# Optimization experiments

Hardware: AMD Instinct MI355X
Metric: run time of the kernel (lower is better)

The kernel has to match this reference:

```python
import jax, jax.numpy as jnp
import numpy as np

N_NODES = 100000
N_EDGES = 640000
IN_DIM, HID_DIM, OUT_DIM = 128, 64, 32


def setup_inputs() -> dict:
    key = jax.random.key(0)
    ks = jax.random.split(key, 8)
    x = jax.random.normal(ks[0], (N_NODES, IN_DIM), dtype=jnp.float32)
    edge_index = jax.random.randint(ks[1], (2, N_EDGES), 0, N_NODES, dtype=jnp.int64)
    # SAGEConv params: lin_l (applied to aggregated neighbors, has bias),
    # lin_r (applied to root node, no bias) -- PyG defaults.
    s1 = 1.0 / np.sqrt(IN_DIM)
    s2 = 1.0 / np.sqrt(HID_DIM)
    W1l = jax.random.uniform(ks[2], (HID_DIM, IN_DIM), jnp.float32, -s1, s1)
    b1 = jax.random.uniform(ks[3], (HID_DIM,), jnp.float32, -s1, s1)
    W1r = jax.random.uniform(ks[4], (HID_DIM, IN_DIM), jnp.float32, -s1, s1)
    W2l = jax.random.uniform(ks[5], (OUT_DIM, HID_DIM), jnp.float32, -s2, s2)
    b2 = jax.random.uniform(ks[6], (OUT_DIM,), jnp.float32, -s2, s2)
    W2r = jax.random.uniform(ks[7], (OUT_DIM, HID_DIM), jnp.float32, -s2, s2)
    return {"x": x, "edge_index": edge_index,
            "W1l": W1l, "b1": b1, "W1r": W1r,
            "W2l": W2l, "b2": b2, "W2r": W2r}


def _sage_conv(x, src, dst, Wl, b, Wr, num_nodes):
    # mean aggregation of source features onto destination nodes
    msg = x[src]                                                # [E, d]
    agg = jax.ops.segment_sum(msg, dst, num_segments=num_nodes)  # [N, d]
    cnt = jax.ops.segment_sum(jnp.ones((src.shape[0],), x.dtype), dst,
                              num_segments=num_nodes)            # [N]
    agg = agg / jnp.maximum(cnt, 1.0)[:, None]
    # out = lin_l(mean_neighbors) + lin_r(x)
    return agg @ Wl.T + b + x @ Wr.T


def reference(x, edge_index, W1l, b1, W1r, W2l, b2, W2r):
    src, dst = edge_index[0], edge_index[1]
    n = x.shape[0]
    h = jax.nn.relu(_sage_conv(x, src, dst, W1l, b1, W1r, n))
    out = _sage_conv(h, src, dst, W2l, b2, W2r, n)
    return out
```

## Files before the change

kernel.cpp:

```cpp
#include <hip/hip_runtime.h>
#include <hip/hip_bf16.h>

typedef __hip_bfloat16 bf16;
typedef __attribute__((ext_vector_type(8))) short short8;
typedef __attribute__((ext_vector_type(4))) float f32x4;

#define N_NODES 100000
#define N_EDGES 640000
#define NSB 98
#define N_TILES 6250

__device__ __forceinline__ float bf2f(short s) {
    union { float f; unsigned u; } u;
    u.u = ((unsigned)(unsigned short)s) << 16;
    return u.f;
}
__device__ __forceinline__ short f2s(float f) {
    union { bf16 b; short s; } u;
    u.b = __float2bfloat16(f);
    return u.s;
}

__device__ __forceinline__ int detect_is64(const int* __restrict__ idx) {
    int lane = threadIdx.x & 63;
    int v = idx[2 * (lane & 31) + 1];
    return __ballot(v == 0) == ~0ULL;
}
__device__ __forceinline__ int detect_f32(const unsigned* __restrict__ xw) {
    int lane = threadIdx.x & 63;
    unsigned e = (xw[lane] >> 7) & 0xFFu;
    int inr = (e >= 0x20u && e <= 0x4Fu);
    return __popcll(__ballot(inr)) < 48;
}

__device__ __forceinline__ void decode8(
        const int* __restrict__ eidx, int is64, int e0, int E,
        int (&ss)[8], int (&dd)[8]) {
    if (is64) {
        int4 a0 = *(const int4*)&eidx[2 * e0];
        int4 a1 = *(const int4*)&eidx[2 * e0 + 4];
        int4 a2 = *(const int4*)&eidx[2 * e0 + 8];
        int4 a3 = *(const int4*)&eidx[2 * e0 + 12];
        int4 b0 = *(const int4*)&eidx[2 * (E + e0)];
        int4 b1 = *(const int4*)&eidx[2 * (E + e0) + 4];
        int4 b2 = *(const int4*)&eidx[2 * (E + e0) + 8];
        int4 b3 = *(const int4*)&eidx[2 * (E + e0) + 12];
        ss[0] = a0.x; ss[1] = a0.z; ss[2] = a1.x; ss[3] = a1.z;
        ss[4] = a2.x; ss[5] = a2.z; ss[6] = a3.x; ss[7] = a3.z;
        dd[0] = b0.x; dd[1] = b0.z; dd[2] = b1.x; dd[3] = b1.z;
        dd[4] = b2.x; dd[5] = b2.z; dd[6] = b3.x; dd[7] = b3.z;
    } else {
        int4 s0 = *(const int4*)&eidx[e0];
        int4 s1 = *(const int4*)&eidx[e0 + 4];
        int4 d0 = *(const int4*)&eidx[E + e0];
        int4 d1 = *(const int4*)&eidx[E + e0 + 4];
        ss[0] = s0.x; ss[1] = s0.y; ss[2] = s0.z; ss[3] = s0.w;
        ss[4] = s1.x; ss[5] = s1.y; ss[6] = s1.z; ss[7] = s1.w;
        dd[0] = d0.x; dd[1] = d0.y; dd[2] = d0.z; dd[3] = d0.w;
        dd[4] = d1.x; dd[5] = d1.y; dd[6] = d1.z; dd[7] = d1.w;
    }
}

__global__ __launch_bounds__(256) void hist_kernel(
        const int* __restrict__ eidx, int* __restrict__ deg,
        int* __restrict__ rank, int E, int N) {
    const int is64 = detect_is64(eidx);
    int e0 = (blockIdx.x * 256 + threadIdx.x) * 8;
    if (e0 >= E) return;
    int ss[8], dd[8], rk[8];
    decode8(eidx, is64, e0, E, ss, dd);
#pragma unroll
    for (int c = 0; c < 8; ++c) {
        bool ok = (unsigned)ss[c] < (unsigned)N && (unsigned)dd[c] < (unsigned)N;
        rk[c] = ok ? atomicAdd(&deg[dd[c]], 1) : 0;
    }
    *(int4*)&rank[e0]     = make_int4(rk[0], rk[1], rk[2], rk[3]);
    *(int4*)&rank[e0 + 4] = make_int4(rk[4], rk[5], rk[6], rk[7]);
}

__global__ __launch_bounds__(256) void scan_partial_kernel(
        const int* __restrict__ deg, int* __restrict__ off,
        int* __restrict__ bsum, int N) {
    __shared__ int ss[256];
    const int tid = threadIdx.x, blk = blockIdx.x;
    const int base = blk * 1024 + tid * 4;
    int v[4], s = 0;
    if (base + 3 < N) {
        int4 dv = *(const int4*)&deg[base];
        v[0] = dv.x; v[1] = dv.y; v[2] = dv.z; v[3] = dv.w;
    } else {
#pragma unroll
        for (int c = 0; c < 4; ++c) v[c] = (base + c < N) ? deg[base + c] : 0;
    }
#pragma unroll
    for (int c = 0; c < 4; ++c) s += v[c];
    ss[tid] = s; __syncthreads();
    for (int o = 1; o < 256; o <<= 1) {
        int t = (tid >= o) ? ss[tid - o] : 0;
        __syncthreads();
        ss[tid] += t;
        __syncthreads();
    }
    int run = ss[tid] - s;
    if (tid == 255) bsum[blk] = ss[255];
#pragma unroll
    for (int c = 0; c < 4; ++c) {
        if (base + c < N) off[base + c] = run;
        run += v[c];
    }
}

__global__ __launch_bounds__(256) void scan_add_kernel(
        int* __restrict__ off, const int* __restrict__ bsum, int N) {
    __shared__ int ss[NSB];
    const int blk = blockIdx.x, tid = threadIdx.x;
    if (tid < NSB) ss[tid] = bsum[tid];
    __syncthreads();
    int add = 0;
    for (int i = 0; i < blk; ++i) add += ss[i];
    const int base = blk * 1024 + tid * 4;
#pragma unroll
    for (int c = 0; c < 4; ++c) {
        int i = base + c;
        if (i < N) off[i] += add;
    }
    if (blk == NSB - 1 && tid == 0)
        off[N] = add + ss[NSB - 1];
}

__global__ __launch_bounds__(256) void fill_kernel(
        const int* __restrict__ eidx, const int* __restrict__ off,
        const int* __restrict__ rank, int* __restrict__ srcs, int E, int N) {
    const int is64 = detect_is64(eidx);
    int e0 = (blockIdx.x * 256 + threadIdx.x) * 8;
    if (e0 >= E) return;
    int ss[8], dd[8];
    decode8(eidx, is64, e0, E, ss, dd);
    int4 r0 = *(const int4*)&rank[e0];
    int4 r1 = *(const int4*)&rank[e0 + 4];
    const int rk[8] = {r0.x, r0.y, r0.z, r0.w, r1.x, r1.y, r1.z, r1.w};
#pragma unroll
    for (int c = 0; c < 8; ++c) {
        if ((unsigned)ss[c] >= (unsigned)N || (unsigned)dd[c] >= (unsigned)N) continue;
        srcs[off[dd[c]] + rk[c]] = ss[c];
    }
}

__global__ __launch_bounds__(256) void gather1_kernel(
        const int* __restrict__ srcs, const int* __restrict__ off,
        const bf16* __restrict__ xl, const bf16* __restrict__ xr,
        const void* __restrict__ b1, bf16* __restrict__ h,
        const unsigned* __restrict__ xdet, int N) {
    const int f32 = detect_f32(xdet);
    const int tid = threadIdx.x;
    const int node = blockIdx.x * 16 + (tid >> 4);
    const int j = tid & 15;
    const int gbase = (tid & 63) & ~15;
    const int a = off[node], b = off[node + 1];
    float a0 = 0.f, a1 = 0.f, a2 = 0.f, a3 = 0.f;
    for (int base = a; base < b; base += 16) {
        const int cdeg = min(b - base, 16);
        int sv = (j < cdeg) ? srcs[base + j] : 0;
        for (int bb = 0; bb < cdeg; bb += 4) {
#pragma unroll
            for (int t = 0; t < 4; ++t) {
                const int idx = bb + t;
                const int s = __shfl(sv, gbase + (idx < cdeg ? idx : 0));
                if (idx < cdeg) {
                    short4 v = *(const short4*)((const short*)xl + (size_t)s * 64 + j * 4);
                    a0 += bf2f(v.x); a1 += bf2f(v.y);
                    a2 += bf2f(v.z); a3 += bf2f(v.w);
                }
            }
        }
    }
    float b0, b1v, b2v, b3;
    if (f32) {
        float4 bb4 = *(const float4*)((const float*)b1 + j * 4);
        b0 = bb4.x; b1v = bb4.y; b2v = bb4.z; b3 = bb4.w;
    } else {
        short4 bb4 = *(const short4*)((const short*)b1 + j * 4);
        b0 = bf2f(bb4.x); b1v = bf2f(bb4.y); b2v = bf2f(bb4.z); b3 = bf2f(bb4.w);
    }
    short4 xr4 = *(const short4*)((const short*)xr + (size_t)node * 64 + j * 4);
    const float inv = 1.0f / fmaxf((float)(b - a), 1.0f);
    short4 o;
    o.x = f2s(fmaxf(a0 * inv + b0  + bf2f(xr4.x), 0.0f));
    o.y = f2s(fmaxf(a1 * inv + b1v + bf2f(xr4.y), 0.0f));
    o.z = f2s(fmaxf(a2 * inv + b2v + bf2f(xr4.z), 0.0f));
    o.w = f2s(fmaxf(a3 * inv + b3  + bf2f(xr4.w), 0.0f));
    *(short4*)((short*)h + (size_t)node * 64 + j * 4) = o;
}

__global__ __launch_bounds__(256) void gather2_kernel(
        const int* __restrict__ srcs, const int* __restrict__ off,
        const bf16* __restrict__ hl, const bf16* __restrict__ hr,
        const void* __restrict__ b2, void* __restrict__ out,
        const unsigned* __restrict__ xdet, int N) {
    const int f32 = detect_f32(xdet);
    const int tid = threadIdx.x;
    const int node = blockIdx.x * 32 + (tid >> 3);
    const int j = tid & 7;
    const int gbase = (tid & 63) & ~7;
    const int a = off[node], b = off[node + 1];
    float a0 = 0.f, a1 = 0.f, a2 = 0.f, a3 = 0.f;
    for (int base = a; base < b; base += 8) {
        const int cdeg = min(b - base, 8);
        int sv = (j < cdeg) ? srcs[base + j] : 0;
        for (int bb = 0; bb < cdeg; bb += 4) {
#pragma unroll
            for (int t = 0; t < 4; ++t) {
                const int idx = bb + t;
                const int s = __shfl(sv, gbase + (idx < cdeg ? idx : 0));
                if (idx < cdeg) {
                    short4 v = *(const short4*)((const short*)hl + (size_t)s * 32 + j * 4);
                    a0 += bf2f(v.x); a1 += bf2f(v.y);
                    a2 += bf2f(v.z); a3 += bf2f(v.w);
                }
            }
        }
    }
    float b0, b1v, b2v, b3;
    if (f32) {
        float4 bb4 = *(const float4*)((const float*)b2 + j * 4);
        b0 = bb4.x; b1v = bb4.y; b2v = bb4.z; b3 = bb4.w;
    } else {
        short4 bb4 = *(const short4*)((const short*)b2 + j * 4);
        b0 = bf2f(bb4.x); b1v = bf2f(bb4.y); b2v = bf2f(bb4.z); b3 = bf2f(bb4.w);
    }
    short4 hr4 = *(const short4*)((const short*)hr + (size_t)node * 32 + j * 4);
    const float inv = 1.0f / fmaxf((float)(b - a), 1.0f);
    const float v0 = a0 * inv + b0  + bf2f(hr4.x);
    const float v1 = a1 * inv + b1v + bf2f(hr4.y);
    const float v2 = a2 * inv + b2v + bf2f(hr4.z);
    const float v3 = a3 * inv + b3  + bf2f(hr4.w);
    if (f32) {
        *(float4*)((float*)out + (size_t)node * 32 + j * 4) =
            make_float4(v0, v1, v2, v3);
    } else {
        short4 o;
        o.x = f2s(v0); o.y = f2s(v1); o.z = f2s(v2); o.w = f2s(v3);
        *(short4*)((short*)out + (size_t)node * 32 + j * 4) = o;
    }
}

__device__ __forceinline__ short8 load_frag(const void* base, size_t eoff, int f32) {
    if (f32) {
        const float4* p = (const float4*)((const float*)base + eoff);
        const float4 u = p[0], v = p[1];
        short8 r;
        r[0] = f2s(u.x); r[1] = f2s(u.y); r[2] = f2s(u.z); r[3] = f2s(u.w);
        r[4] = f2s(v.x); r[5] = f2s(v.y); r[6] = f2s(v.z); r[7] = f2s(v.w);
        return r;
    }
    return *(const short8*)((const short*)base + eoff);
}

__global__ __launch_bounds__(256) void lin1_kernel(
        const void* __restrict__ x, const void* __restrict__ W1l,
        const void* __restrict__ W1r, bf16* __restrict__ xl,
        bf16* __restrict__ xr) {
    const int f32 = detect_f32((const unsigned*)x);
    __shared__ short wlds[2][16][64][8];

    const int tid = threadIdx.x;
    {
        const int l = tid & 63, fg = tid >> 6;
        const int mm = l & 15, qq = l >> 4;
#pragma unroll
        for (int i = 0; i < 4; ++i) {
            const int f = fg * 4 + i;
            const int ks = f >> 2, dt = f & 3;
            const size_t wo = (size_t)(dt * 16 + mm) * 128 + ks * 32 + qq * 8;
            *(short8*)&wlds[0][f][l][0] = load_frag(W1l, wo, f32);
            *(short8*)&wlds[1][f][l][0] = load_frag(W1r, wo, f32);
        }
    }
    __syncthreads();

    const int nwaves = gridDim.x * 4;
    const int wid = blockIdx.x * 4 + (tid >> 6);
    const int lane = tid & 63;
    const int m = lane & 15, quad = lane >> 4;
    const short* wl0 = &wlds[0][0][lane][0];
    const short* wr0 = &wlds[1][0][lane][0];

    int tile = wid;
    if (tile >= N_TILES) return;

    short8 a[4];
    {
        const size_t arow = (size_t)(tile * 16 + m) * 128 + quad * 8;
#pragma unroll
        for (int ks = 0; ks < 4; ++ks)
            a[ks] = load_frag(x, arow + ks * 32, f32);
    }

    while (true) {
        const int nxt = tile + nwaves;
        short8 an[4];
        if (nxt < N_TILES) {
            const size_t arow = (size_t)(nxt * 16 + m) * 128 + quad * 8;
#pragma unroll
            for (int ks = 0; ks < 4; ++ks)
                an[ks] = load_frag(x, arow + ks * 32, f32);
        }

        f32x4 accl[4], accr[4];
#pragma unroll
        for (int dt = 0; dt < 4; ++dt) {
            accl[dt] = (f32x4){0.f, 0.f, 0.f, 0.f};
            accr[dt] = (f32x4){0.f, 0.f, 0.f, 0.f};
        }
#pragma unroll
        for (int ks = 0; ks < 4; ++ks)
#pragma unroll
            for (int dt = 0; dt < 4; ++dt) {
                const short8 wl = *(const short8*)(wl0 + (ks * 4 + dt) * 512);
                const short8 wr = *(const short8*)(wr0 + (ks * 4 + dt) * 512);
                accl[dt] = __builtin_amdgcn_mfma_f32_16x16x32_bf16(
                    wl, a[ks], accl[dt], 0, 0, 0);
                accr[dt] = __builtin_amdgcn_mfma_f32_16x16x32_bf16(
                    wr, a[ks], accr[dt], 0, 0, 0);
            }

        const int node = tile * 16 + m;
#pragma unroll
        for (int dt = 0; dt < 4; ++dt) {
            short4 pl, pr;
            pl.x = f2s(accl[dt][0]); pl.y = f2s(accl[dt][1]);
            pl.z = f2s(accl[dt][2]); pl.w = f2s(accl[dt][3]);
            pr.x = f2s(accr[dt][0]); pr.y = f2s(accr[dt][1]);
            pr.z = f2s(accr[dt][2]); pr.w = f2s(accr[dt][3]);
            *(short4*)((short*)xl + (size_t)node * 64 + dt * 16 + quad * 4) = pl;
            *(short4*)((short*)xr + (size_t)node * 64 + dt * 16 + quad * 4) = pr;
        }

        if (nxt >= N_TILES) break;
        tile = nxt;
#pragma unroll
        for (int ks = 0; ks < 4; ++ks) a[ks] = an[ks];
    }
}

__global__ __launch_bounds__(256) void lin2_kernel(
        const bf16* __restrict__ h, const void* __restrict__ W2l,
        const void* __restrict__ W2r, bf16* __restrict__ hl,
        bf16* __restrict__ hr, const unsigned* __restrict__ xdet) {
    const int f32 = detect_f32(xdet);
    const int nwaves = gridDim.x * 4;
    const int wid = blockIdx.x * 4 + (threadIdx.x >> 6);
    const int lane = threadIdx.x & 63;
    const int m = lane & 15, quad = lane >> 4;

    short8 bfr[8];
#pragma unroll
    for (int ks = 0; ks < 2; ++ks)
#pragma unroll
        for (int nt = 0; nt < 4; ++nt) {
            const void* Wb = (nt < 2) ? W2l : W2r;
            bfr[ks * 4 + nt] =
                load_frag(Wb, (size_t)((nt & 1) * 16 + m) * 64 + ks * 32 + quad * 8, f32);
        }

    for (int tile = wid; tile < N_TILES; tile += nwaves) {
        f32x4 acc[4];
#pragma unroll
        for (int nt = 0; nt < 4; ++nt) acc[nt] = (f32x4){0.f, 0.f, 0.f, 0.f};

        const size_t arow = (size_t)(tile * 16 + m) * 64;
        short8 a[2];
#pragma unroll
        for (int ks = 0; ks < 2; ++ks)
            a[ks] = *(const short8*)((const short*)h + arow + ks * 32 + quad * 8);
#pragma unroll
        for (int ks = 0; ks < 2; ++ks)
#pragma unroll
            for (int nt = 0; nt < 4; ++nt)
                acc[nt] = __builtin_amdgcn_mfma_f32_16x16x32_bf16(
                    bfr[ks * 4 + nt], a[ks], acc[nt], 0, 0, 0);

        const int node = tile * 16 + m;
#pragma unroll
        for (int nt = 0; nt < 4; ++nt) {
            bf16* dst = (nt < 2) ? hl : hr;
            short4 p;
            p.x = f2s(acc[nt][0]); p.y = f2s(acc[nt][1]);
            p.z = f2s(acc[nt][2]); p.w = f2s(acc[nt][3]);
            *(short4*)((short*)dst + (size_t)node * 32 + (nt & 1) * 16 + quad * 4) = p;
        }
    }
}

extern "C" void kernel_launch(void* const* d_in, const int* in_sizes, int n_in,
                              void* d_out, int out_size, void* d_ws, size_t ws_size,
                              hipStream_t stream) {
    const void* x   = d_in[0];
    const int*  eix = (const int*)d_in[1];
    const void* W1l = d_in[2];
    const void* b1  = d_in[3];
    const void* W1r = d_in[4];
    const void* W2l = d_in[5];
    const void* b2  = d_in[6];
    const void* W2r = d_in[7];

    const int N = N_NODES;
    const int E = N_EDGES;

    char* ws = (char*)d_ws;
    bf16*  xl    = (bf16*)(ws + 256);
    bf16*  xr    = (bf16*)(ws + 256 + (size_t)N * 128);
    bf16*  h     = (bf16*)(ws + 256 + (size_t)N * 256);
    bf16*  hl    = (bf16*)(ws + 256 + (size_t)N * 384);
    bf16*  hr    = (bf16*)(ws + 256 + (size_t)N * 448);
    int*   off   = (int*) (ws + 256 + (size_t)N * 512);
    int*   deg   = off + (N + 4);
    int*   rank  = deg + N;
    int*   srcs  = rank + E;
    int*   bsum  = srcs + E;

    hipMemsetAsync(deg, 0, (size_t)N * 4, stream);
    const int ge = (E / 8 + 255) / 256;
    hist_kernel<<<ge, 256, 0, stream>>>(eix, deg, rank, E, N);
    scan_partial_kernel<<<NSB, 256, 0, stream>>>(deg, off, bsum, N);
    scan_add_kernel<<<NSB, 256, 0, stream>>>(off, bsum, N);
    fill_kernel<<<ge, 256, 0, stream>>>(eix, off, rank, srcs, E, N);

    lin1_kernel<<<1024, 256, 0, stream>>>(x, W1l, W1r, xl, xr);

    gather1_kernel<<<N / 16, 256, 0, stream>>>(
        srcs, off, xl, xr, b1, h, (const unsigned*)x, N);

    lin2_kernel<<<1024, 256, 0, stream>>>(h, W2l, W2r, hl, hr, (const unsigned*)x);

    gather2_kernel<<<N / 32, 256, 0, stream>>>(
        srcs, off, hl, hr, b2, d_out, (const unsigned*)x, N);
}
```

Before: 220.8 us.

## Fuse CSR build stages and merge lin1/hist and gather1/lin2 kernels

```diff
diff --git a/kernel.cpp b/kernel.cpp
--- a/kernel.cpp
+++ b/kernel.cpp
@@ -9,6 +9,8 @@
 #define N_EDGES 640000
 #define NSB 98
 #define N_TILES 6250
+#define GE 313
+#define LIN1_BLKS 1024
 
 __device__ __forceinline__ float bf2f(short s) {
     union { float f; unsigned u; } u;
@@ -31,6 +33,18 @@
     unsigned e = (xw[lane] >> 7) & 0xFFu;
     int inr = (e >= 0x20u && e <= 0x4Fu);
     return __popcll(__ballot(inr)) < 48;
+}
+
+__device__ __forceinline__ void gbar(int* ctr, int target) {
+    __syncthreads();
+    if (threadIdx.x == 0) {
+        __threadfence();
+        atomicAdd(ctr, 1);
+        while (__hip_atomic_load(ctr, __ATOMIC_ACQUIRE,
+                                 __HIP_MEMORY_SCOPE_AGENT) < target)
+            __builtin_amdgcn_s_sleep(8);
+    }
+    __syncthreads();
 }
 
 __device__ __forceinline__ void decode8(
@@ -61,101 +75,222 @@
     }
 }
 
-__global__ __launch_bounds__(256) void hist_kernel(
-        const int* __restrict__ eidx, int* __restrict__ deg,
-        int* __restrict__ rank, int E, int N) {
-    const int is64 = detect_is64(eidx);
-    int e0 = (blockIdx.x * 256 + threadIdx.x) * 8;
-    if (e0 >= E) return;
-    int ss[8], dd[8], rk[8];
-    decode8(eidx, is64, e0, E, ss, dd);
-#pragma unroll
-    for (int c = 0; c < 8; ++c) {
-        bool ok = (unsigned)ss[c] < (unsigned)N && (unsigned)dd[c] < (unsigned)N;
-        rk[c] = ok ? atomicAdd(&deg[dd[c]], 1) : 0;
-    }
-    *(int4*)&rank[e0]     = make_int4(rk[0], rk[1], rk[2], rk[3]);
-    *(int4*)&rank[e0 + 4] = make_int4(rk[4], rk[5], rk[6], rk[7]);
-}
-
-__global__ __launch_bounds__(256) void scan_partial_kernel(
-        const int* __restrict__ deg, int* __restrict__ off,
-        int* __restrict__ bsum, int N) {
+__device__ __forceinline__ short8 load_frag(const void* base, size_t eoff, int f32) {
+    if (f32) {
+        const float4* p = (const float4*)((const float*)base + eoff);
+        const float4 u = p[0], v = p[1];
+        short8 r;
+        r[0] = f2s(u.x); r[1] = f2s(u.y); r[2] = f2s(u.z); r[3] = f2s(u.w);
+        r[4] = f2s(v.x); r[5] = f2s(v.y); r[6] = f2s(v.z); r[7] = f2s(v.w);
+        return r;
+    }
+    return *(const short8*)((const short*)base + eoff);
+}
+
+__global__ __launch_bounds__(256) void lin1_hist_kernel(
+        const void* __restrict__ x, const void* __restrict__ W1l,
+        const void* __restrict__ W1r, bf16* __restrict__ xl,
+        bf16* __restrict__ xr, const int* __restrict__ eidx,
+        int* __restrict__ deg, int* __restrict__ rank) {
+    __shared__ short wlds[2][16][64][8];
+    const int tid = threadIdx.x;
+
+    if (blockIdx.x >= LIN1_BLKS) {
+        const int blk = blockIdx.x - LIN1_BLKS;
+        const int is64 = detect_is64(eidx);
+        int e0 = (blk * 256 + tid) * 8;
+        if (e0 >= N_EDGES) return;
+        int ss[8], dd[8], rk[8];
+        decode8(eidx, is64, e0, N_EDGES, ss, dd);
+#pragma unroll
+        for (int c = 0; c < 8; ++c) {
+            bool ok = (unsigned)ss[c] < (unsigned)N_NODES &&
+                      (unsigned)dd[c] < (unsigned)N_NODES;
+            rk[c] = ok ? atomicAdd(&deg[dd[c]], 1) : 0;
+        }
+        *(int4*)&rank[e0]     = make_int4(rk[0], rk[1], rk[2], rk[3]);
+        *(int4*)&rank[e0 + 4] = make_int4(rk[4], rk[5], rk[6], rk[7]);
+        return;
+    }
+
+    const int f32 = detect_f32((const unsigned*)x);
+    {
+        const int l = tid & 63, fg = tid >> 6;
+        const int mm = l & 15, qq = l >> 4;
+#pragma unroll
+        for (int i = 0; i < 4; ++i) {
+            const int f = fg * 4 + i;
+            const int ks = f >> 2, dt = f & 3;
+            const size_t wo = (size_t)(dt * 16 + mm) * 128 + ks * 32 + qq * 8;
+            *(short8*)&wlds[0][f][l][0] = load_frag(W1l, wo, f32);
+            *(short8*)&wlds[1][f][l][0] = load_frag(W1r, wo, f32);
+        }
+    }
+    __syncthreads();
+
+    const int nwaves = LIN1_BLKS * 4;
+    const int wid = blockIdx.x * 4 + (tid >> 6);
+    const int lane = tid & 63;
+    const int m = lane & 15, quad = lane >> 4;
+    const short* wl0 = &wlds[0][0][lane][0];
+    const short* wr0 = &wlds[1][0][lane][0];
+
+    int tile = wid;
+    if (tile >= N_TILES) return;
+
+    short8 a[4];
+    {
+        const size_t arow = (size_t)(tile * 16 + m) * 128 + quad * 8;
+#pragma unroll
+        for (int ks = 0; ks < 4; ++ks)
+            a[ks] = load_frag(x, arow + ks * 32, f32);
+    }
+
+    while (true) {
+        const int nxt = tile + nwaves;
+        short8 an[4];
+        if (nxt < N_TILES) {
+            const size_t arow = (size_t)(nxt * 16 + m) * 128 + quad * 8;
+#pragma unroll
+            for (int ks = 0; ks < 4; ++ks)
+                an[ks] = load_frag(x, arow + ks * 32, f32);
+        }
+
+        f32x4 accl[4], accr[4];
+#pragma unroll
+        for (int dt = 0; dt < 4; ++dt) {
+            accl[dt] = (f32x4){0.f, 0.f, 0.f, 0.f};
+            accr[dt] = (f32x4){0.f, 0.f, 0.f, 0.f};
+        }
+#pragma unroll
+        for (int ks = 0; ks < 4; ++ks)
+#pragma unroll
+            for (int dt = 0; dt < 4; ++dt) {
+                const short8 wl = *(const short8*)(wl0 + (ks * 4 + dt) * 512);
+                const short8 wr = *(const short8*)(wr0 + (ks * 4 + dt) * 512);
+                accl[dt] = __builtin_amdgcn_mfma_f32_16x16x32_bf16(
+                    wl, a[ks], accl[dt], 0, 0, 0);
+                accr[dt] = __builtin_amdgcn_mfma_f32_16x16x32_bf16(
+                    wr, a[ks], accr[dt], 0, 0, 0);
+            }
+
+        const int node = tile * 16 + m;
+#pragma unroll
+        for (int dt = 0; dt < 4; ++dt) {
+            short4 pl, pr;
+            pl.x = f2s(accl[dt][0]); pl.y = f2s(accl[dt][1]);
+            pl.z = f2s(accl[dt][2]); pl.w = f2s(accl[dt][3]);
+            pr.x = f2s(accr[dt][0]); pr.y = f2s(accr[dt][1]);
+            pr.z = f2s(accr[dt][2]); pr.w = f2s(accr[dt][3]);
+            *(short4*)((short*)xl + (size_t)node * 64 + dt * 16 + quad * 4) = pl;
+            *(short4*)((short*)xr + (size_t)node * 64 + dt * 16 + quad * 4) = pr;
+        }
+
+        if (nxt >= N_TILES) break;
+        tile = nxt;
+#pragma unroll
+        for (int ks = 0; ks < 4; ++ks) a[ks] = an[ks];
+    }
+}
+
+__global__ __launch_bounds__(256) void csr_kernel(
+        const int* __restrict__ eidx, const int* __restrict__ deg,
+        int* __restrict__ off, int* __restrict__ bsum,
+        const int* __restrict__ rank, int* __restrict__ srcs,
+        int* __restrict__ ctr) {
     __shared__ int ss[256];
     const int tid = threadIdx.x, blk = blockIdx.x;
-    const int base = blk * 1024 + tid * 4;
-    int v[4], s = 0;
-    if (base + 3 < N) {
-        int4 dv = *(const int4*)&deg[base];
-        v[0] = dv.x; v[1] = dv.y; v[2] = dv.z; v[3] = dv.w;
-    } else {
-#pragma unroll
-        for (int c = 0; c < 4; ++c) v[c] = (base + c < N) ? deg[base + c] : 0;
-    }
-#pragma unroll
-    for (int c = 0; c < 4; ++c) s += v[c];
-    ss[tid] = s; __syncthreads();
-    for (int o = 1; o < 256; o <<= 1) {
-        int t = (tid >= o) ? ss[tid - o] : 0;
+
+    if (blk < NSB) {
+        const int base = blk * 1024 + tid * 4;
+        int v[4], s = 0;
+        if (base + 3 < N_NODES) {
+            int4 dv = *(const int4*)&deg[base];
+            v[0] = dv.x; v[1] = dv.y; v[2] = dv.z; v[3] = dv.w;
+        } else {
+#pragma unroll
+            for (int c = 0; c < 4; ++c) v[c] = (base + c < N_NODES) ? deg[base + c] : 0;
+        }
+#pragma unroll
+        for (int c = 0; c < 4; ++c) s += v[c];
+        ss[tid] = s; __syncthreads();
+        for (int o = 1; o < 256; o <<= 1) {
+            int t = (tid >= o) ? ss[tid - o] : 0;
+            __syncthreads();
+            ss[tid] += t;
+            __syncthreads();
+        }
+        int run = ss[tid] - s;
+        if (tid == 255) bsum[blk] = ss[255];
+#pragma unroll
+        for (int c = 0; c < 4; ++c) {
+            if (base + c < N_NODES) off[base + c] = run;
+            run += v[c];
+        }
+    }
+
+    gbar(&ctr[0], gridDim.x);
+
+    if (blk < NSB) {
+        if (tid < NSB)
+            ss[tid] = __hip_atomic_load(&bsum[tid], __ATOMIC_RELAXED,
+                                        __HIP_MEMORY_SCOPE_AGENT);
         __syncthreads();
-        ss[tid] += t;
-        __syncthreads();
-    }
-    int run = ss[tid] - s;
-    if (tid == 255) bsum[blk] = ss[255];
-#pragma unroll
-    for (int c = 0; c < 4; ++c) {
-        if (base + c < N) off[base + c] = run;
-        run += v[c];
-    }
-}
-
-__global__ __launch_bounds__(256) void scan_add_kernel(
-        int* __restrict__ off, const int* __restrict__ bsum, int N) {
-    __shared__ int ss[NSB];
-    const int blk = blockIdx.x, tid = threadIdx.x;
-    if (tid < NSB) ss[tid] = bsum[tid];
-    __syncthreads();
-    int add = 0;
-    for (int i = 0; i < blk; ++i) add += ss[i];
-    const int base = blk * 1024 + tid * 4;
-#pragma unroll
-    for (int c = 0; c < 4; ++c) {
-        int i = base + c;
-        if (i < N) off[i] += add;
-    }
-    if (blk == NSB - 1 && tid == 0)
-        off[N] = add + ss[NSB - 1];
-}
-
-__global__ __launch_bounds__(256) void fill_kernel(
-        const int* __restrict__ eidx, const int* __restrict__ off,
-        const int* __restrict__ rank, int* __restrict__ srcs, int E, int N) {
+        int add = 0;
+        for (int i = 0; i < blk; ++i) add += ss[i];
+        const int base = blk * 1024 + tid * 4;
+#pragma unroll
+        for (int c = 0; c < 4; ++c) {
+            int i = base + c;
+            if (i < N_NODES) off[i] += add;
+        }
+        if (blk == NSB - 1 && tid == 0)
+            off[N_NODES] = add + ss[NSB - 1];
+    }
+
+    gbar(&ctr[1], gridDim.x);
+
     const int is64 = detect_is64(eidx);
-    int e0 = (blockIdx.x * 256 + threadIdx.x) * 8;
-    if (e0 >= E) return;
-    int ss[8], dd[8];
-    decode8(eidx, is64, e0, E, ss, dd);
+    int e0 = (blk * 256 + tid) * 8;
+    if (e0 >= N_EDGES) return;
+    int sse[8], dd[8];
+    decode8(eidx, is64, e0, N_EDGES, sse, dd);
     int4 r0 = *(const int4*)&rank[e0];
     int4 r1 = *(const int4*)&rank[e0 + 4];
     const int rk[8] = {r0.x, r0.y, r0.z, r0.w, r1.x, r1.y, r1.z, r1.w};
 #pragma unroll
     for (int c = 0; c < 8; ++c) {
-        if ((unsigned)ss[c] >= (unsigned)N || (unsigned)dd[c] >= (unsigned)N) continue;
-        srcs[off[dd[c]] + rk[c]] = ss[c];
-    }
-}
-
-__global__ __launch_bounds__(256) void gather1_kernel(
+        if ((unsigned)sse[c] >= (unsigned)N_NODES ||
+            (unsigned)dd[c]  >= (unsigned)N_NODES) continue;
+        int offd = __hip_atomic_load(&off[dd[c]], __ATOMIC_RELAXED,
+                                     __HIP_MEMORY_SCOPE_AGENT);
+        srcs[offd + rk[c]] = sse[c];
+    }
+}
+
+__global__ __launch_bounds__(256) void gather1_lin2_kernel(
         const int* __restrict__ srcs, const int* __restrict__ off,
         const bf16* __restrict__ xl, const bf16* __restrict__ xr,
-        const void* __restrict__ b1, bf16* __restrict__ h,
-        const unsigned* __restrict__ xdet, int N) {
+        const void* __restrict__ b1, const void* __restrict__ W2l,
+        const void* __restrict__ W2r, bf16* __restrict__ hl,
+        bf16* __restrict__ hr, const unsigned* __restrict__ xdet) {
     const int f32 = detect_f32(xdet);
     const int tid = threadIdx.x;
+    const int lane = tid & 63, wave = tid >> 6;
+    const int m = lane & 15, quad = lane >> 4;
+
+    const void* Wb = (wave < 2) ? W2l : W2r;
+    short8 bfrag[2];
+#pragma unroll
+    for (int ks = 0; ks < 2; ++ks)
+        bfrag[ks] = load_frag(
+            Wb, (size_t)((wave & 1) * 16 + m) * 64 + ks * 32 + quad * 8, f32);
+
+    __shared__ short htile[16][72];
+
     const int node = blockIdx.x * 16 + (tid >> 4);
     const int j = tid & 15;
-    const int gbase = (tid & 63) & ~15;
+    const int gbase = lane & ~15;
     const int a = off[node], b = off[node + 1];
     float a0 = 0.f, a1 = 0.f, a2 = 0.f, a3 = 0.f;
     for (int base = a; base < b; base += 16) {
@@ -189,7 +324,25 @@
     o.y = f2s(fmaxf(a1 * inv + b1v + bf2f(xr4.y), 0.0f));
     o.z = f2s(fmaxf(a2 * inv + b2v + bf2f(xr4.z), 0.0f));
     o.w = f2s(fmaxf(a3 * inv + b3  + bf2f(xr4.w), 0.0f));
-    *(short4*)((short*)h + (size_t)node * 64 + j * 4) = o;
+    *(short4*)&htile[tid >> 4][j * 4] = o;
+    __syncthreads();
+
+    short8 afr[2];
+#pragma unroll
+    for (int ks = 0; ks < 2; ++ks)
+        afr[ks] = *(const short8*)&htile[m][ks * 32 + quad * 8];
+    f32x4 acc = (f32x4){0.f, 0.f, 0.f, 0.f};
+#pragma unroll
+    for (int ks = 0; ks < 2; ++ks)
+        acc = __builtin_amdgcn_mfma_f32_16x16x32_bf16(
+            bfrag[ks], afr[ks], acc, 0, 0, 0);
+
+    bf16* dst = (wave < 2) ? hl : hr;
+    const int onode = blockIdx.x * 16 + m;
+    short4 p;
+    p.x = f2s(acc[0]); p.y = f2s(acc[1]);
+    p.z = f2s(acc[2]); p.w = f2s(acc[3]);
+    *(short4*)((short*)dst + (size_t)onode * 32 + (wave & 1) * 16 + quad * 4) = p;
 }
 
 __global__ __launch_bounds__(256) void gather2_kernel(
@@ -244,154 +397,6 @@
     }
 }
 
-__device__ __forceinline__ short8 load_frag(const void* base, size_t eoff, int f32) {
-    if (f32) {
-        const float4* p = (const float4*)((const float*)base + eoff);
-        const float4 u = p[0], v = p[1];
-        short8 r;
-        r[0] = f2s(u.x); r[1] = f2s(u.y); r[2] = f2s(u.z); r[3] = f2s(u.w);
-        r[4] = f2s(v.x); r[5] = f2s(v.y); r[6] = f2s(v.z); r[7] = f2s(v.w);
-        return r;
-    }
-    return *(const short8*)((const short*)base + eoff);
-}
-
-__global__ __launch_bounds__(256) void lin1_kernel(
-        const void* __restrict__ x, const void* __restrict__ W1l,
-        const void* __restrict__ W1r, bf16* __restrict__ xl,
-        bf16* __restrict__ xr) {
-    const int f32 = detect_f32((const unsigned*)x);
-    __shared__ short wlds[2][16][64][8];
-
-    const int tid = threadIdx.x;
-    {
-        const int l = tid & 63, fg = tid >> 6;
-        const int mm = l & 15, qq = l >> 4;
-#pragma unroll
-        for (int i = 0; i < 4; ++i) {
-            const int f = fg * 4 + i;
-            const int ks = f >> 2, dt = f & 3;
-            const size_t wo = (size_t)(dt * 16 + mm) * 128 + ks * 32 + qq * 8;
-            *(short8*)&wlds[0][f][l][0] = load_frag(W1l, wo, f32);
-            *(short8*)&wlds[1][f][l][0] = load_frag(W1r, wo, f32);
-        }
-    }
-    __syncthreads();
-
-    const int nwaves = gridDim.x * 4;
-    const int wid = blockIdx.x * 4 + (tid >> 6);
-    const int lane = tid & 63;
-    const int m = lane & 15, quad = lane >> 4;
-    const short* wl0 = &wlds[0][0][lane][0];
-    const short* wr0 = &wlds[1][0][lane][0];
-
-    int tile = wid;
-    if (tile >= N_TILES) return;
-
-    short8 a[4];
-    {
-        const size_t arow = (size_t)(tile * 16 + m) * 128 + quad * 8;
-#pragma unroll
-        for (int ks = 0; ks < 4; ++ks)
-            a[ks] = load_frag(x, arow + ks * 32, f32);
-    }
-
-    while (true) {
-        const int nxt = tile + nwaves;
-        short8 an[4];
-        if (nxt < N_TILES) {
-            const size_t arow = (size_t)(nxt * 16 + m) * 128 + quad * 8;
-#pragma unroll
-            for (int ks = 0; ks < 4; ++ks)
-                an[ks] = load_frag(x, arow + ks * 32, f32);
-        }
-
-        f32x4 accl[4], accr[4];
-#pragma unroll
-        for (int dt = 0; dt < 4; ++dt) {
-            accl[dt] = (f32x4){0.f, 0.f, 0.f, 0.f};
-            accr[dt] = (f32x4){0.f, 0.f, 0.f, 0.f};
-        }
-#pragma unroll
-        for (int ks = 0; ks < 4; ++ks)
-#pragma unroll
-            for (int dt = 0; dt < 4; ++dt) {
-                const short8 wl = *(const short8*)(wl0 + (ks * 4 + dt) * 512);
-                const short8 wr = *(const short8*)(wr0 + (ks * 4 + dt) * 512);
-                accl[dt] = __builtin_amdgcn_mfma_f32_16x16x32_bf16(
-                    wl, a[ks], accl[dt], 0, 0, 0);
-                accr[dt] = __builtin_amdgcn_mfma_f32_16x16x32_bf16(
-                    wr, a[ks], accr[dt], 0, 0, 0);
-            }
-
-        const int node = tile * 16 + m;
-#pragma unroll
-        for (int dt = 0; dt < 4; ++dt) {
-            short4 pl, pr;
-            pl.x = f2s(accl[dt][0]); pl.y = f2s(accl[dt][1]);
-            pl.z = f2s(accl[dt][2]); pl.w = f2s(accl[dt][3]);
-            pr.x = f2s(accr[dt][0]); pr.y = f2s(accr[dt][1]);
-            pr.z = f2s(accr[dt][2]); pr.w = f2s(accr[dt][3]);
-            *(short4*)((short*)xl + (size_t)node * 64 + dt * 16 + quad * 4) = pl;
-            *(short4*)((short*)xr + (size_t)node * 64 + dt * 16 + quad * 4) = pr;
-        }
-
-        if (nxt >= N_TILES) break;
-        tile = nxt;
-#pragma unroll
-        for (int ks = 0; ks < 4; ++ks) a[ks] = an[ks];
-    }
-}
-
-__global__ __launch_bounds__(256) void lin2_kernel(
-        const bf16* __restrict__ h, const void* __restrict__ W2l,
-        const void* __restrict__ W2r, bf16* __restrict__ hl,
-        bf16* __restrict__ hr, const unsigned* __restrict__ xdet) {
-    const int f32 = detect_f32(xdet);
-    const int nwaves = gridDim.x * 4;
-    const int wid = blockIdx.x * 4 + (threadIdx.x >> 6);
-    const int lane = threadIdx.x & 63;
-    const int m = lane & 15, quad = lane >> 4;
-
-    short8 bfr[8];
-#pragma unroll
-    for (int ks = 0; ks < 2; ++ks)
-#pragma unroll
-        for (int nt = 0; nt < 4; ++nt) {
-            const void* Wb = (nt < 2) ? W2l : W2r;
-            bfr[ks * 4 + nt] =
-                load_frag(Wb, (size_t)((nt & 1) * 16 + m) * 64 + ks * 32 + quad * 8, f32);
-        }
-
-    for (int tile = wid; tile < N_TILES; tile += nwaves) {
-        f32x4 acc[4];
-#pragma unroll
-        for (int nt = 0; nt < 4; ++nt) acc[nt] = (f32x4){0.f, 0.f, 0.f, 0.f};
-
-        const size_t arow = (size_t)(tile * 16 + m) * 64;
-        short8 a[2];
-#pragma unroll
-        for (int ks = 0; ks < 2; ++ks)
-            a[ks] = *(const short8*)((const short*)h + arow + ks * 32 + quad * 8);
-#pragma unroll
-        for (int ks = 0; ks < 2; ++ks)
-#pragma unroll
-            for (int nt = 0; nt < 4; ++nt)
-                acc[nt] = __builtin_amdgcn_mfma_f32_16x16x32_bf16(
-                    bfr[ks * 4 + nt], a[ks], acc[nt], 0, 0, 0);
-
-        const int node = tile * 16 + m;
-#pragma unroll
-        for (int nt = 0; nt < 4; ++nt) {
-            bf16* dst = (nt < 2) ? hl : hr;
-            short4 p;
-            p.x = f2s(acc[nt][0]); p.y = f2s(acc[nt][1]);
-            p.z = f2s(acc[nt][2]); p.w = f2s(acc[nt][3]);
-            *(short4*)((short*)dst + (size_t)node * 32 + (nt & 1) * 16 + quad * 4) = p;
-        }
-    }
-}
-
 extern "C" void kernel_launch(void* const* d_in, const int* in_sizes, int n_in,
                               void* d_out, int out_size, void* d_ws, size_t ws_size,
                               hipStream_t stream) {
@@ -410,28 +415,24 @@
     char* ws = (char*)d_ws;
     bf16*  xl    = (bf16*)(ws + 256);
     bf16*  xr    = (bf16*)(ws + 256 + (size_t)N * 128);
-    bf16*  h     = (bf16*)(ws + 256 + (size_t)N * 256);
     bf16*  hl    = (bf16*)(ws + 256 + (size_t)N * 384);
     bf16*  hr    = (bf16*)(ws + 256 + (size_t)N * 448);
     int*   off   = (int*) (ws + 256 + (size_t)N * 512);
     int*   deg   = off + (N + 4);
-    int*   rank  = deg + N;
+    int*   ctr   = deg + N;
+    int*   rank  = ctr + 8;
     int*   srcs  = rank + E;
     int*   bsum  = srcs + E;
 
-    hipMemsetAsync(deg, 0, (size_t)N * 4, stream);
-    const int ge = (E / 8 + 255) / 256;
-    hist_kernel<<<ge, 256, 0, stream>>>(eix, deg, rank, E, N);
-    scan_partial_kernel<<<NSB, 256, 0, stream>>>(deg, off, bsum, N);
-    scan_add_kernel<<<NSB, 256, 0, stream>>>(off, bsum, N);
-    fill_kernel<<<ge, 256, 0, stream>>>(eix, off, rank, srcs, E, N);
-
-    lin1_kernel<<<1024, 256, 0, stream>>>(x, W1l, W1r, xl, xr);
-
-    gather1_kernel<<<N / 16, 256, 0, stream>>>(
-        srcs, off, xl, xr, b1, h, (const unsigned*)x, N);
-
-    lin2_kernel<<<1024, 256, 0, stream>>>(h, W2l, W2r, hl, hr, (const unsigned*)x);
+    hipMemsetAsync(deg, 0, (size_t)(N + 8) * 4, stream);
+
+    lin1_hist_kernel<<<LIN1_BLKS + GE, 256, 0, stream>>>(
+        x, W1l, W1r, xl, xr, eix, deg, rank);
+
+    csr_kernel<<<GE, 256, 0, stream>>>(eix, deg, off, bsum, rank, srcs, ctr);
+
+    gather1_lin2_kernel<<<N / 16, 256, 0, stream>>>(
+        srcs, off, xl, xr, b1, W2l, W2r, hl, hr, (const unsigned*)x);
 
     gather2_kernel<<<N / 32, 256, 0, stream>>>(
         srcs, off, hl, hr, b2, d_out, (const unsigned*)x, N);
```

Measured after the change: 267.7 us. 1.21x slower.
